# Performance work log

Hardware: AMD Instinct MI355X
Metric: run time of the kernel (lower is better)

## Reference

```python
import jax, jax.numpy as jnp
import numpy as np

N_PER_G = 6            # EEG channels per graph (complete graph incl. self-loops)
ALPHA = 0.5
BETA1 = float(np.log(1.0 / 1 + 1.0))  # GCN2Conv layer=1, lambda=1
BETA2 = float(np.log(1.0 / 2 + 1.0))  # GCN2Conv layer=2
BN_EPS = 1e-5


def setup_inputs() -> dict:
    key = jax.random.key(0)
    ks = jax.random.split(key, 10)
    G = 400_000
    N = G * N_PER_G          # 2.4M nodes
    E = G * N_PER_G * N_PER_G  # 14.4M edges (complete graph per EEG window)

    x = jax.random.normal(ks[0], (N, 6), dtype=jnp.float32)
    edge_weights = jax.random.uniform(ks[1], (E,), dtype=jnp.float32)

    # Batched complete-graph connectivity (numpy, structured)
    base = (np.arange(G, dtype=np.int64) * N_PER_G)
    ls = np.repeat(np.arange(N_PER_G), N_PER_G)   # local src
    ld = np.tile(np.arange(N_PER_G), N_PER_G)     # local dst
    src = jnp.asarray((base[:, None] + ls[None, :]).reshape(-1).astype(np.int32))
    dst = jnp.asarray((base[:, None] + ld[None, :]).reshape(-1).astype(np.int32))

    s6 = 1.0 / np.sqrt(6.0)
    W1 = jax.random.normal(ks[2], (6, 6), dtype=jnp.float32) * s6
    b1 = jnp.zeros((6,), dtype=jnp.float32)
    W2 = jax.random.normal(ks[3], (6, 6), dtype=jnp.float32) * s6
    b2 = jnp.zeros((6,), dtype=jnp.float32)
    gamma = jnp.ones((6,), dtype=jnp.float32)
    beta_bn = jnp.zeros((6,), dtype=jnp.float32)
    fcW1 = jax.random.normal(ks[4], (6, 10), dtype=jnp.float32) * s6   # xavier-ish
    fcb1 = jnp.zeros((10,), dtype=jnp.float32)
    fcW2 = jax.random.normal(ks[5], (10, 2), dtype=jnp.float32) * (1.0 / np.sqrt(10.0))
    fcb2 = jnp.zeros((2,), dtype=jnp.float32)

    return {"x": x, "edge_weights": edge_weights, "W1": W1, "b1": b1,
            "W2": W2, "b2": b2, "gamma": gamma, "beta_bn": beta_bn,
            "fcW1": fcW1, "fcb1": fcb1, "fcW2": fcW2, "fcb2": fcb2,
            "src": src, "dst": dst, "num_graphs": G}


def _gcn2_conv(feat, feat0, W, b, beta, edge_weights, src, dst, norm, n_nodes):
    # DGL GCN2Conv: sym-norm edge-weighted aggregation, identity mixing, proj mixing
    h = feat * norm                                   # [N,6]
    msg = h[src] * edge_weights[:, None]              # [E,6] gather
    agg = jax.ops.segment_sum(msg, dst, num_segments=n_nodes)  # [N,6] scatter-add
    h = agg * norm
    h = (1.0 - ALPHA) * h + ALPHA * feat0
    return (1.0 - beta) * h + beta * (h @ W) + b


def reference(x, edge_weights, W1, b1, W2, b2, gamma, beta_bn,
              fcW1, fcb1, fcW2, fcb2, src, dst, num_graphs):
    N = x.shape[0]
    # symmetric normalization from in-degrees (clamped to 1)
    deg = jax.ops.segment_sum(jnp.ones_like(edge_weights), dst, num_segments=N)
    norm = jax.lax.rsqrt(jnp.maximum(deg, 1.0))[:, None]  # [N,1]

    h = jax.nn.leaky_relu(_gcn2_conv(x, x, W1, b1, BETA1, edge_weights, src, dst, norm, N))
    h = _gcn2_conv(h, h, W2, b2, BETA2, edge_weights, src, dst, norm, N)

    # BatchNorm1d over nodes (training-mode batch statistics)
    mean = jnp.mean(h, axis=0)
    var = jnp.mean(jnp.square(h - mean), axis=0)
    h = (h - mean) * jax.lax.rsqrt(var + BN_EPS) * gamma + beta_bn
    h = jax.nn.leaky_relu(h)

    # SumPooling per graph (node i belongs to graph i // 6)
    gid = jnp.arange(N, dtype=jnp.int32) // N_PER_G
    pooled = jax.ops.segment_sum(h, gid, num_segments=num_graphs)  # [G,6]

    out = jax.nn.leaky_relu(pooled @ fcW1 + fcb1)  # dropout is identity at inference
    out = out @ fcW2 + fcb2                        # [G,2]
    return out
```

## Files before the change

### kernel.cpp

```cpp
#include <hip/hip_runtime.h>
#include <cstddef>
#include <cstdint>

#define NSLOT 64
#define ALPHA 0.5f
#define B1f   0.6931471805599453f
#define B2f   0.4054651081081644f

__device__ __forceinline__ float lrelu(float v) { return v >= 0.0f ? v : 0.01f * v; }

__device__ __forceinline__ float gc(const float4* a, int idx) {
  const float4 v = a[idx >> 2];
  const int c = idx & 3;
  return c == 0 ? v.x : (c == 1 ? v.y : (c == 2 ? v.z : v.w));
}

__device__ __forceinline__ unsigned pkbf(float a, float b) {
  unsigned ua = __float_as_uint(a), ub = __float_as_uint(b);
  ua += 0x7FFFu + ((ua >> 16) & 1u);
  ub += 0x7FFFu + ((ub >> 16) & 1u);
  return (ua >> 16) | (ub & 0xFFFF0000u);
}

__device__ __forceinline__ void gl_lds16(const float4* gp, float4* lbase) {
#if __has_builtin(__builtin_amdgcn_global_load_lds)
  __builtin_amdgcn_global_load_lds(
      (const __attribute__((address_space(1))) void*)(const void*)gp,
      (__attribute__((address_space(3))) void*)(void*)lbase, 16, 0, 0);
#else
  ((float4*)lbase)[threadIdx.x & 63] = *gp;
#endif
}

__device__ __forceinline__ void compute_h2(const float4* X, const float4* Wt,
                                           const float* __restrict__ gW1,
                                           const float* __restrict__ gb1,
                                           const float* __restrict__ gW2,
                                           const float* __restrict__ gb2,
                                           float h2[36]) {
  float t[36];
#pragma unroll
  for (int j = 0; j < 6; ++j)
#pragma unroll
    for (int f = 0; f < 6; ++f) {
      float a = 0.f;
#pragma unroll
      for (int i = 0; i < 6; ++i) a = fmaf(gc(Wt, i * 6 + j), gc(X, i * 6 + f), a);
      t[j * 6 + f] = fmaf(a, ALPHA * (1.f / 6.f), ALPHA * gc(X, j * 6 + f));
    }
  float h1[36];
#pragma unroll
  for (int j = 0; j < 6; ++j)
#pragma unroll
    for (int f = 0; f < 6; ++f) {
      float a = 0.f;
#pragma unroll
      for (int k = 0; k < 6; ++k) a = fmaf(t[j * 6 + k], gW1[k * 6 + f], a);
      h1[j * 6 + f] = lrelu(fmaf(B1f, a, fmaf(1.f - B1f, t[j * 6 + f], gb1[f])));
    }
#pragma unroll
  for (int j = 0; j < 6; ++j)
#pragma unroll
    for (int f = 0; f < 6; ++f) {
      float a = 0.f;
#pragma unroll
      for (int i = 0; i < 6; ++i) a = fmaf(gc(Wt, i * 6 + j), h1[i * 6 + f], a);
      t[j * 6 + f] = fmaf(a, ALPHA * (1.f / 6.f), ALPHA * h1[j * 6 + f]);
    }
#pragma unroll
  for (int j = 0; j < 6; ++j)
#pragma unroll
    for (int f = 0; f < 6; ++f) {
      float a = 0.f;
#pragma unroll
      for (int k = 0; k < 6; ++k) a = fmaf(t[j * 6 + k], gW2[k * 6 + f], a);
      h2[j * 6 + f] = fmaf(B2f, a, fmaf(1.f - B2f, t[j * 6 + f], gb2[f]));
    }
}

__device__ __forceinline__ void bn_coeffs(const float* __restrict__ wsred,
                                          const float* __restrict__ gGamma,
                                          const float* __restrict__ gBeta,
                                          float invN, int lane,
                                          float sc[6], float sh[6]) {
  float st[12];
  const float4* p = reinterpret_cast<const float4*>(wsred) + (size_t)lane * 3;
  float4 a = p[0], b = p[1], c4 = p[2];
  st[0] = a.x;  st[1] = a.y;  st[2]  = a.z;  st[3]  = a.w;
  st[4] = b.x;  st[5] = b.y;  st[6]  = b.z;  st[7]  = b.w;
  st[8] = c4.x; st[9] = c4.y; st[10] = c4.z; st[11] = c4.w;
#pragma unroll
  for (int k = 0; k < 12; ++k)
#pragma unroll
    for (int o = 32; o >= 1; o >>= 1) st[k] += __shfl_xor(st[k], (unsigned)o, 64);
#pragma unroll
  for (int f = 0; f < 6; ++f) {
    float mean = st[f] * invN;
    float var  = st[6 + f] * invN - mean * mean;
    float s    = rsqrtf(var + 1e-5f) * gGamma[f];
    sc[f] = s;
    sh[f] = gBeta[f] - mean * s;
  }
}

__device__ __forceinline__ void pool_fc_out(const float h2[36],
                                            const float sc[6], const float sh[6],
                                            const float* __restrict__ fcW1,
                                            const float* __restrict__ fcb1,
                                            const float* __restrict__ fcW2,
                                            const float* __restrict__ fcb2,
                                            float2* __restrict__ out, int g) {
  float pooled[6] = {0.f, 0.f, 0.f, 0.f, 0.f, 0.f};
#pragma unroll
  for (int j = 0; j < 6; ++j)
#pragma unroll
    for (int f = 0; f < 6; ++f)
      pooled[f] += lrelu(fmaf(h2[j * 6 + f], sc[f], sh[f]));
  float p1[10];
#pragma unroll
  for (int m = 0; m < 10; ++m) {
    float a = fcb1[m];
#pragma unroll
    for (int f = 0; f < 6; ++f) a = fmaf(pooled[f], fcW1[f * 10 + m], a);
    p1[m] = lrelu(a);
  }
  float o0 = fcb2[0], o1 = fcb2[1];
#pragma unroll
  for (int m = 0; m < 10; ++m) {
    o0 = fmaf(p1[m], fcW2[m * 2 + 0], o0);
    o1 = fmaf(p1[m], fcW2[m * 2 + 1], o1);
  }
  out[g] = make_float2(o0, o1);
}

__global__ __launch_bounds__(256, 2) void gcn2_pass1(
    const float* __restrict__ x, const float* __restrict__ ew,
    const float* __restrict__ gW1, const float* __restrict__ gb1,
    const float* __restrict__ gW2, const float* __restrict__ gb2,
    float* __restrict__ wsred, unsigned* __restrict__ h2ws,
    int G, int useWs) {
  __shared__ float4 sbuf[4][2][576];

  const int tid  = threadIdx.x;
  const int lane = tid & 63;
  const int wid  = tid >> 6;
  const int wgid = blockIdx.x * 4 + wid;
  const int wstr = gridDim.x * 4;
  const int nch  = (G + 31) >> 5;

  const float4* x4 = reinterpret_cast<const float4*>(x);
  const float4* w4 = reinterpret_cast<const float4*>(ew);
  const long fmax4 = (long)G * 9 - 1;

  uint4* wsA = reinterpret_cast<uint4*>(h2ws);
  uint2* wsB = reinterpret_cast<uint2*>(h2ws + (size_t)16 * G);

  float s[6]  = {0.f, 0.f, 0.f, 0.f, 0.f, 0.f};
  float ss[6] = {0.f, 0.f, 0.f, 0.f, 0.f, 0.f};

  int c = wgid;
  if (c < nch) {
    int cur = 0;
#pragma unroll
    for (int k = 0; k < 9; ++k) {
      const int F = k * 64 + lane;
      long fi = (F < 288) ? ((long)c * 288 + F) : ((long)c * 288 + F - 288);
      if (fi > fmax4) fi = fmax4;
      gl_lds16(((F < 288) ? x4 : w4) + fi, &sbuf[wid][0][k * 64]);
    }
    for (;;) {
      const int cn = c + wstr;
      const bool hn = cn < nch;
      if (hn) {
#pragma unroll
        for (int k = 0; k < 9; ++k) {
          const int F = k * 64 + lane;
          long fi = (F < 288) ? ((long)cn * 288 + F) : ((long)cn * 288 + F - 288);
          if (fi > fmax4) fi = fmax4;
          gl_lds16(((F < 288) ? x4 : w4) + fi, &sbuf[wid][cur ^ 1][k * 64]);
        }
      }
      __builtin_amdgcn_sched_barrier(0);
      if (hn) { __asm__ volatile("s_waitcnt vmcnt(9)" ::: "memory"); }
      else    { __asm__ volatile("s_waitcnt vmcnt(0)" ::: "memory"); }
      __builtin_amdgcn_sched_barrier(0);

      if (lane < 32) {
        const int g = c * 32 + lane;
        if (g < G) {
          const float4* bx = &sbuf[wid][cur][lane * 9];
          const float4* bw = &sbuf[wid][cur][288 + lane * 9];
          float h2[36];
          compute_h2(bx, bw, gW1, gb1, gW2, gb2, h2);
          if (useWs) {
            unsigned d[18];
#pragma unroll
            for (int k = 0; k < 18; ++k) d[k] = pkbf(h2[2 * k], h2[2 * k + 1]);
            wsA[(size_t)0 * G + g] = make_uint4(d[0],  d[1],  d[2],  d[3]);
            wsA[(size_t)1 * G + g] = make_uint4(d[4],  d[5],  d[6],  d[7]);
            wsA[(size_t)2 * G + g] = make_uint4(d[8],  d[9],  d[10], d[11]);
            wsA[(size_t)3 * G + g] = make_uint4(d[12], d[13], d[14], d[15]);
            wsB[g]                 = make_uint2(d[16], d[17]);
          }
#pragma unroll
          for (int f = 0; f < 6; ++f)
#pragma unroll
            for (int j = 0; j < 6; ++j) {
              float v = h2[j * 6 + f];
              s[f] += v;
              ss[f] = fmaf(v, v, ss[f]);
            }
        }
      }
      if (!hn) break;
      __asm__ volatile("s_waitcnt lgkmcnt(0)" ::: "memory");
      __builtin_amdgcn_sched_barrier(0);
      c = cn;
      cur ^= 1;
    }
  }

#pragma unroll
  for (int f = 0; f < 6; ++f)
#pragma unroll
    for (int o = 32; o >= 1; o >>= 1) {
      s[f]  += __shfl_down(s[f],  (unsigned)o, 64);
      ss[f] += __shfl_down(ss[f], (unsigned)o, 64);
    }
  if (lane == 0) {
    float* p = wsred + (size_t)(wgid & (NSLOT - 1)) * 12;
#pragma unroll
    for (int f = 0; f < 6; ++f) {
      atomicAdd(p + f,     s[f]);
      atomicAdd(p + 6 + f, ss[f]);
    }
  }
}

__global__ __launch_bounds__(256) void gcn2_pass2ws(
    const unsigned* __restrict__ h2ws,
    const float* __restrict__ fcW1, const float* __restrict__ fcb1,
    const float* __restrict__ fcW2, const float* __restrict__ fcb2,
    const float* __restrict__ gGamma, const float* __restrict__ gBeta,
    const float* __restrict__ wsred, float invN,
    float2* __restrict__ out, int G) {
  const int tid  = threadIdx.x;
  const int lane = tid & 63;
  const int g    = blockIdx.x * 256 + tid;

  float sc[6], sh[6];
  bn_coeffs(wsred, gGamma, gBeta, invN, lane, sc, sh);

  if (g >= G) return;

  const uint4* wsA = reinterpret_cast<const uint4*>(h2ws);
  const uint2* wsB = reinterpret_cast<const uint2*>(h2ws + (size_t)16 * G);
  unsigned u[18];
  {
    uint4 a0 = wsA[(size_t)0 * G + g];
    uint4 a1 = wsA[(size_t)1 * G + g];
    uint4 a2 = wsA[(size_t)2 * G + g];
    uint4 a3 = wsA[(size_t)3 * G + g];
    uint2 b0 = wsB[g];
    u[0]=a0.x; u[1]=a0.y; u[2]=a0.z;  u[3]=a0.w;
    u[4]=a1.x; u[5]=a1.y; u[6]=a1.z;  u[7]=a1.w;
    u[8]=a2.x; u[9]=a2.y; u[10]=a2.z; u[11]=a2.w;
    u[12]=a3.x; u[13]=a3.y; u[14]=a3.z; u[15]=a3.w;
    u[16]=b0.x; u[17]=b0.y;
  }
  float h2[36];
#pragma unroll
  for (int d = 0; d < 18; ++d) {
    h2[2 * d]     = __uint_as_float(u[d] << 16);
    h2[2 * d + 1] = __uint_as_float(u[d] & 0xFFFF0000u);
  }
  pool_fc_out(h2, sc, sh, fcW1, fcb1, fcW2, fcb2, out, g);
}

__global__ __launch_bounds__(256) void gcn2_pass2re(
    const float* __restrict__ x, const float* __restrict__ ew,
    const float* __restrict__ gW1, const float* __restrict__ gb1,
    const float* __restrict__ gW2, const float* __restrict__ gb2,
    const float* __restrict__ fcW1, const float* __restrict__ fcb1,
    const float* __restrict__ fcW2, const float* __restrict__ fcb2,
    const float* __restrict__ gGamma, const float* __restrict__ gBeta,
    const float* __restrict__ wsred, float invN,
    float2* __restrict__ out, int G) {
  const int tid  = threadIdx.x;
  const int lane = tid & 63;
  const int g    = blockIdx.x * 256 + tid;

  float sc[6], sh[6];
  bn_coeffs(wsred, gGamma, gBeta, invN, lane, sc, sh);

  if (g >= G) return;

  const float4* px = reinterpret_cast<const float4*>(x)  + (size_t)g * 9;
  const float4* pw = reinterpret_cast<const float4*>(ew) + (size_t)g * 9;
  float4 X[9], Wv[9];
#pragma unroll
  for (int k = 0; k < 9; ++k) X[k]  = px[k];
#pragma unroll
  for (int k = 0; k < 9; ++k) Wv[k] = pw[k];
  float h2[36];
  compute_h2(X, Wv, gW1, gb1, gW2, gb2, h2);
  pool_fc_out(h2, sc, sh, fcW1, fcb1, fcW2, fcb2, out, g);
}

extern "C" void kernel_launch(void* const* d_in, const int* in_sizes, int n_in,
                              void* d_out, int out_size, void* d_ws, size_t ws_size,
                              hipStream_t stream) {
  const float* x     = (const float*)d_in[0];
  const float* ew    = (const float*)d_in[1];
  const float* W1    = (const float*)d_in[2];
  const float* b1    = (const float*)d_in[3];
  const float* W2    = (const float*)d_in[4];
  const float* b2    = (const float*)d_in[5];
  const float* gamma = (const float*)d_in[6];
  const float* beta  = (const float*)d_in[7];
  const float* fcW1  = (const float*)d_in[8];
  const float* fcb1  = (const float*)d_in[9];
  const float* fcW2  = (const float*)d_in[10];
  const float* fcb2  = (const float*)d_in[11];

  const int G = in_sizes[0] / 36;
  const float invN = 1.0f / (6.0f * (float)G);

  float*    wsred = (float*)d_ws;
  unsigned* h2ws  = (unsigned*)((char*)d_ws + 4096);
  const int useWs = (ws_size >= 4096 + (size_t)G * 72) ? 1 : 0;

  hipMemsetAsync(d_ws, 0, NSLOT * 12 * sizeof(float), stream);

  gcn2_pass1<<<512, 256, 0, stream>>>(x, ew, W1, b1, W2, b2,
                                      wsred, h2ws, G, useWs);
  const int grid2 = (G + 255) / 256;
  if (useWs) {
    gcn2_pass2ws<<<grid2, 256, 0, stream>>>(h2ws, fcW1, fcb1, fcW2, fcb2,
                                            gamma, beta, wsred, invN,
                                            (float2*)d_out, G);
  } else {
    gcn2_pass2re<<<grid2, 256, 0, stream>>>(x, ew, W1, b1, W2, b2,
                                            fcW1, fcb1, fcW2, fcb2,
                                            gamma, beta, wsred, invN,
                                            (float2*)d_out, G);
  }
}
```

Baseline: 55.33 us.

## Split per-graph compute across lane pairs and widen pass1 blocks

Pass1 previously used only 32 of 64 lanes per wave, each computing a full graph. Now each graph is split across two lanes, each handling three of the six nodes and exchanging layer-1 activations via a shuffle. The workspace layout becomes half-graph interleaved so pass2 reads contiguous pairs. Blocks grow to 512 threads with 8 waves and a capped grid, which doubles LDS per block and may reduce occupancy or add shuffle overhead.

```diff
diff --git a/kernel.cpp b/kernel.cpp
--- a/kernel.cpp
+++ b/kernel.cpp
@@ -32,12 +32,93 @@
 #endif
 }
 
-__device__ __forceinline__ void compute_h2(const float4* X, const float4* Wt,
-                                           const float* __restrict__ gW1,
-                                           const float* __restrict__ gb1,
-                                           const float* __restrict__ gW2,
-                                           const float* __restrict__ gb2,
-                                           float h2[36]) {
+__device__ __forceinline__ void compute_h2_half(
+    const float4* X, const float4* Wt, int h,
+    const float* __restrict__ gW1, const float* __restrict__ gb1,
+    const float* __restrict__ gW2, const float* __restrict__ gb2,
+    float h2o[18]) {
+  float xv[36], wv[36];
+#pragma unroll
+  for (int k = 0; k < 9; ++k) {
+    float4 v = X[k];
+    xv[4 * k] = v.x; xv[4 * k + 1] = v.y; xv[4 * k + 2] = v.z; xv[4 * k + 3] = v.w;
+  }
+#pragma unroll
+  for (int k = 0; k < 9; ++k) {
+    float4 v = Wt[k];
+    wv[4 * k] = v.x; wv[4 * k + 1] = v.y; wv[4 * k + 2] = v.z; wv[4 * k + 3] = v.w;
+  }
+  float wsel[18], xown[18];
+#pragma unroll
+  for (int i = 0; i < 6; ++i)
+#pragma unroll
+    for (int jr = 0; jr < 3; ++jr)
+      wsel[i * 3 + jr] = h ? wv[i * 6 + 3 + jr] : wv[i * 6 + jr];
+#pragma unroll
+  for (int jr = 0; jr < 3; ++jr)
+#pragma unroll
+    for (int f = 0; f < 6; ++f)
+      xown[jr * 6 + f] = h ? xv[(3 + jr) * 6 + f] : xv[jr * 6 + f];
+
+  float t[18];
+#pragma unroll
+  for (int jr = 0; jr < 3; ++jr)
+#pragma unroll
+    for (int f = 0; f < 6; ++f) {
+      float a = 0.f;
+#pragma unroll
+      for (int i = 0; i < 6; ++i) a = fmaf(wsel[i * 3 + jr], xv[i * 6 + f], a);
+      t[jr * 6 + f] = fmaf(a, 1.f / 12.f, 0.5f * xown[jr * 6 + f]);
+    }
+  float h1o[18];
+#pragma unroll
+  for (int jr = 0; jr < 3; ++jr)
+#pragma unroll
+    for (int f = 0; f < 6; ++f) {
+      float a = 0.f;
+#pragma unroll
+      for (int k = 0; k < 6; ++k) a = fmaf(t[jr * 6 + k], gW1[k * 6 + f], a);
+      h1o[jr * 6 + f] = lrelu(fmaf(B1f, a, fmaf(1.f - B1f, t[jr * 6 + f], gb1[f])));
+    }
+  float h1x[18];
+#pragma unroll
+  for (int q = 0; q < 18; ++q) h1x[q] = __shfl_xor(h1o[q], 1, 64);
+  float hlo[18], hhi[18];
+#pragma unroll
+  for (int q = 0; q < 18; ++q) {
+    hlo[q] = h ? h1x[q] : h1o[q];
+    hhi[q] = h ? h1o[q] : h1x[q];
+  }
+  float t2[18];
+#pragma unroll
+  for (int jr = 0; jr < 3; ++jr)
+#pragma unroll
+    for (int f = 0; f < 6; ++f) {
+      float a = 0.f;
+#pragma unroll
+      for (int ir = 0; ir < 3; ++ir) {
+        a = fmaf(wsel[ir * 3 + jr],       hlo[ir * 6 + f], a);
+        a = fmaf(wsel[(3 + ir) * 3 + jr], hhi[ir * 6 + f], a);
+      }
+      t2[jr * 6 + f] = fmaf(a, 1.f / 12.f, 0.5f * h1o[jr * 6 + f]);
+    }
+#pragma unroll
+  for (int jr = 0; jr < 3; ++jr)
+#pragma unroll
+    for (int f = 0; f < 6; ++f) {
+      float a = 0.f;
+#pragma unroll
+      for (int k = 0; k < 6; ++k) a = fmaf(t2[jr * 6 + k], gW2[k * 6 + f], a);
+      h2o[jr * 6 + f] = fmaf(B2f, a, fmaf(1.f - B2f, t2[jr * 6 + f], gb2[f]));
+    }
+}
+
+__device__ __forceinline__ void compute_h2_full(const float4 X[9], const float4 Wt[9],
+                                                const float* __restrict__ gW1,
+                                                const float* __restrict__ gb1,
+                                                const float* __restrict__ gW2,
+                                                const float* __restrict__ gb2,
+                                                float h2[36]) {
   float t[36];
 #pragma unroll
   for (int j = 0; j < 6; ++j)
@@ -46,7 +127,7 @@
       float a = 0.f;
 #pragma unroll
       for (int i = 0; i < 6; ++i) a = fmaf(gc(Wt, i * 6 + j), gc(X, i * 6 + f), a);
-      t[j * 6 + f] = fmaf(a, ALPHA * (1.f / 6.f), ALPHA * gc(X, j * 6 + f));
+      t[j * 6 + f] = fmaf(a, 1.f / 12.f, 0.5f * gc(X, j * 6 + f));
     }
   float h1[36];
 #pragma unroll
@@ -65,7 +146,7 @@
       float a = 0.f;
 #pragma unroll
       for (int i = 0; i < 6; ++i) a = fmaf(gc(Wt, i * 6 + j), h1[i * 6 + f], a);
-      t[j * 6 + f] = fmaf(a, ALPHA * (1.f / 6.f), ALPHA * h1[j * 6 + f]);
+      t[j * 6 + f] = fmaf(a, 1.f / 12.f, 0.5f * h1[j * 6 + f]);
     }
 #pragma unroll
   for (int j = 0; j < 6; ++j)
@@ -133,27 +214,28 @@
   out[g] = make_float2(o0, o1);
 }
 
-__global__ __launch_bounds__(256, 2) void gcn2_pass1(
+__global__ __launch_bounds__(512, 2) void gcn2_pass1(
     const float* __restrict__ x, const float* __restrict__ ew,
     const float* __restrict__ gW1, const float* __restrict__ gb1,
     const float* __restrict__ gW2, const float* __restrict__ gb2,
     float* __restrict__ wsred, unsigned* __restrict__ h2ws,
     int G, int useWs) {
-  __shared__ float4 sbuf[4][2][576];
+  __shared__ float4 sbuf[8][2][576];
 
   const int tid  = threadIdx.x;
   const int lane = tid & 63;
   const int wid  = tid >> 6;
-  const int wgid = blockIdx.x * 4 + wid;
-  const int wstr = gridDim.x * 4;
+  const int wgid = blockIdx.x * 8 + wid;
+  const int wstr = gridDim.x * 8;
   const int nch  = (G + 31) >> 5;
 
   const float4* x4 = reinterpret_cast<const float4*>(x);
   const float4* w4 = reinterpret_cast<const float4*>(ew);
   const long fmax4 = (long)G * 9 - 1;
 
-  uint4* wsA = reinterpret_cast<uint4*>(h2ws);
-  uint2* wsB = reinterpret_cast<uint2*>(h2ws + (size_t)16 * G);
+  uint4*    s0 = reinterpret_cast<uint4*>(h2ws);
+  uint4*    s1 = reinterpret_cast<uint4*>(h2ws + (size_t)8 * G);
+  unsigned* s2 = h2ws + (size_t)16 * G;
 
   float s[6]  = {0.f, 0.f, 0.f, 0.f, 0.f, 0.f};
   float ss[6] = {0.f, 0.f, 0.f, 0.f, 0.f, 0.f};
@@ -185,28 +267,29 @@
       else    { __asm__ volatile("s_waitcnt vmcnt(0)" ::: "memory"); }
       __builtin_amdgcn_sched_barrier(0);
 
-      if (lane < 32) {
-        const int g = c * 32 + lane;
+      {
+        const int gloc = lane >> 1;
+        const int h    = lane & 1;
+        const int g    = c * 32 + gloc;
         if (g < G) {
-          const float4* bx = &sbuf[wid][cur][lane * 9];
-          const float4* bw = &sbuf[wid][cur][288 + lane * 9];
-          float h2[36];
-          compute_h2(bx, bw, gW1, gb1, gW2, gb2, h2);
+          const float4* bx = &sbuf[wid][cur][gloc * 9];
+          const float4* bw = &sbuf[wid][cur][288 + gloc * 9];
+          float h2o[18];
+          compute_h2_half(bx, bw, h, gW1, gb1, gW2, gb2, h2o);
           if (useWs) {
-            unsigned d[18];
-#pragma unroll
-            for (int k = 0; k < 18; ++k) d[k] = pkbf(h2[2 * k], h2[2 * k + 1]);
-            wsA[(size_t)0 * G + g] = make_uint4(d[0],  d[1],  d[2],  d[3]);
-            wsA[(size_t)1 * G + g] = make_uint4(d[4],  d[5],  d[6],  d[7]);
-            wsA[(size_t)2 * G + g] = make_uint4(d[8],  d[9],  d[10], d[11]);
-            wsA[(size_t)3 * G + g] = make_uint4(d[12], d[13], d[14], d[15]);
-            wsB[g]                 = make_uint2(d[16], d[17]);
+            unsigned d[9];
+#pragma unroll
+            for (int k = 0; k < 9; ++k) d[k] = pkbf(h2o[2 * k], h2o[2 * k + 1]);
+            const size_t p = (size_t)c * 64 + lane;
+            s0[p] = make_uint4(d[0], d[1], d[2], d[3]);
+            s1[p] = make_uint4(d[4], d[5], d[6], d[7]);
+            s2[p] = d[8];
           }
 #pragma unroll
           for (int f = 0; f < 6; ++f)
 #pragma unroll
-            for (int j = 0; j < 6; ++j) {
-              float v = h2[j * 6 + f];
+            for (int jr = 0; jr < 3; ++jr) {
+              float v = h2o[jr * 6 + f];
               s[f] += v;
               ss[f] = fmaf(v, v, ss[f]);
             }
@@ -253,27 +336,28 @@
 
   if (g >= G) return;
 
-  const uint4* wsA = reinterpret_cast<const uint4*>(h2ws);
-  const uint2* wsB = reinterpret_cast<const uint2*>(h2ws + (size_t)16 * G);
-  unsigned u[18];
-  {
-    uint4 a0 = wsA[(size_t)0 * G + g];
-    uint4 a1 = wsA[(size_t)1 * G + g];
-    uint4 a2 = wsA[(size_t)2 * G + g];
-    uint4 a3 = wsA[(size_t)3 * G + g];
-    uint2 b0 = wsB[g];
-    u[0]=a0.x; u[1]=a0.y; u[2]=a0.z;  u[3]=a0.w;
-    u[4]=a1.x; u[5]=a1.y; u[6]=a1.z;  u[7]=a1.w;
-    u[8]=a2.x; u[9]=a2.y; u[10]=a2.z; u[11]=a2.w;
-    u[12]=a3.x; u[13]=a3.y; u[14]=a3.z; u[15]=a3.w;
-    u[16]=b0.x; u[17]=b0.y;
-  }
+  const uint4* s0 = reinterpret_cast<const uint4*>(h2ws);
+  const uint4* s1 = reinterpret_cast<const uint4*>(h2ws + (size_t)8 * G);
+  const uint2* s2 = reinterpret_cast<const uint2*>(h2ws + (size_t)16 * G);
+  uint4 A0 = s0[(size_t)2 * g], A1 = s0[(size_t)2 * g + 1];
+  uint4 B0 = s1[(size_t)2 * g], B1 = s1[(size_t)2 * g + 1];
+  uint2 C  = s2[g];
+
+  unsigned dh[2][9];
+  dh[0][0]=A0.x; dh[0][1]=A0.y; dh[0][2]=A0.z; dh[0][3]=A0.w;
+  dh[0][4]=B0.x; dh[0][5]=B0.y; dh[0][6]=B0.z; dh[0][7]=B0.w; dh[0][8]=C.x;
+  dh[1][0]=A1.x; dh[1][1]=A1.y; dh[1][2]=A1.z; dh[1][3]=A1.w;
+  dh[1][4]=B1.x; dh[1][5]=B1.y; dh[1][6]=B1.z; dh[1][7]=B1.w; dh[1][8]=C.y;
+
   float h2[36];
 #pragma unroll
-  for (int d = 0; d < 18; ++d) {
-    h2[2 * d]     = __uint_as_float(u[d] << 16);
-    h2[2 * d + 1] = __uint_as_float(u[d] & 0xFFFF0000u);
-  }
+  for (int h = 0; h < 2; ++h)
+#pragma unroll
+    for (int q = 0; q < 9; ++q) {
+      unsigned u = dh[h][q];
+      h2[h * 18 + 2 * q]     = __uint_as_float(u << 16);
+      h2[h * 18 + 2 * q + 1] = __uint_as_float(u & 0xFFFF0000u);
+    }
   pool_fc_out(h2, sc, sh, fcW1, fcb1, fcW2, fcb2, out, g);
 }
 
@@ -303,7 +387,7 @@
 #pragma unroll
   for (int k = 0; k < 9; ++k) Wv[k] = pw[k];
   float h2[36];
-  compute_h2(X, Wv, gW1, gb1, gW2, gb2, h2);
+  compute_h2_full(X, Wv, gW1, gb1, gW2, gb2, h2);
   pool_fc_out(h2, sc, sh, fcW1, fcb1, fcW2, fcb2, out, g);
 }
 
@@ -332,8 +416,13 @@
 
   hipMemsetAsync(d_ws, 0, NSLOT * 12 * sizeof(float), stream);
 
-  gcn2_pass1<<<512, 256, 0, stream>>>(x, ew, W1, b1, W2, b2,
-                                      wsred, h2ws, G, useWs);
+  const int nch = (G + 31) / 32;
+  int blocks = (nch + 7) / 8;
+  if (blocks > 256) blocks = 256;
+  if (blocks < 1)   blocks = 1;
+
+  gcn2_pass1<<<blocks, 512, 0, stream>>>(x, ew, W1, b1, W2, b2,
+                                         wsred, h2ws, G, useWs);
   const int grid2 = (G + 255) / 256;
   if (useWs) {
     gcn2_pass2ws<<<grid2, 256, 0, stream>>>(h2ws, fcW1, fcb1, fcW2, fcb2,
```

New measurement: 55.74 us. No clear change (+0.7%).
